# Optimization experiments

Measured on AMD Instinct MI355X. Metric: run time of the kernel, lower is better.

## Reference

```python
import jax, jax.numpy as jnp
import numpy as np

H, W = 128, 192          # image size (height, width) after imsz swap
K = 31                   # weight_sl (local window size)
T = K // 2               # replicate padding
C_FEAT = 64              # feat_dim
FFT_ROWS, FFT_COLS = 32, 48  # rect fft mask (after '48,32' swap)


def fft_rect(x):
    # rfft2 low-pass rectangular mask, exactly as fft_ifft with 'rect'.
    f = jnp.fft.rfft2(x)
    rows = jnp.arange(f.shape[-2])[:, None] < FFT_ROWS
    cols = jnp.arange(f.shape[-1])[None, :] < FFT_COLS
    f = f * (rows & cols)
    return jnp.fft.irfft2(f, s=x.shape[-2:])


def make_grid():
    t = float(T)  # weight_sl//2 with downsample_factor=1
    xs = jnp.linspace(-t, t, K)
    gx, gy = jnp.meshgrid(xs, xs, indexing='ij')
    return jnp.stack((gx, gy), axis=-1)  # [K,K,2]


def local_corr(src, tgt):
    # src, tgt: [C,H,W] -> cost volume [H,W,K,K]
    sp = jnp.pad(src, ((0, 0), (T, T), (T, T)), mode='edge')  # replicate pad
    rows = []
    for k in range(K):  # fixed structural loop over window rows
        sl = sp[:, k:k + H, :]  # [C,H,W+2T]
        win = jax.lax.conv_general_dilated_patches(sl[None], (1, K), (1, 1), 'VALID')[0]
        win = win.reshape(C_FEAT, K, H, W)  # [C,l,H,W]
        rows.append(jnp.einsum('chw,clhw->hwl', tgt, win))
    return jnp.stack(rows, axis=-2)  # [H,W,k,l]


def setup_inputs() -> dict:
    key = jax.random.key(0)
    k1, k2, k3 = jax.random.split(key, 3)
    fill_val = (1.0 / C_FEAT) ** 0.5
    feats = fill_val + 0.02 * jax.random.normal(k1, (1, 2, C_FEAT, H, W), jnp.float32)
    in_frames = jax.random.normal(k2, (1, 1, 3, H, W), jnp.float32)
    tgt_frames = jax.random.normal(k3, (1, 1, 3, H, W), jnp.float32)
    return {"in_frames": in_frames, "tgt_frames": tgt_frames, "feats": feats, "temp": 10}


def reference(in_frames, tgt_frames, feats, temp):
    # src_idx=0, tgt_idx=1, single-frame 'feats' path
    src = fft_rect(feats[0, 0])  # [C,H,W]
    tgt = fft_rect(feats[0, 1])
    # bilinear interpolate(scale_factor=1) is identity
    src = src / jnp.linalg.norm(src, axis=0, keepdims=True)
    tgt = tgt / jnp.linalg.norm(tgt, axis=0, keepdims=True)
    w = local_corr(src, tgt) * temp                       # [H,W,K,K]
    w = jax.nn.softmax(w.reshape(H, W, K * K), axis=-1).reshape(H, W, K, K)

    # windowed average of in_frames with per-pixel softmax weights
    xp = jnp.pad(in_frames[0, 0], ((0, 0), (T, T), (T, T)), mode='edge')
    patches = jax.lax.conv_general_dilated_patches(xp[None], (K, K), (1, 1), 'VALID')[0]
    patches = patches.reshape(3, K, K, H, W)              # [C,k,l,H,W]
    out = jnp.einsum('cklhw,hwkl->chw', patches, w)[None, None]  # [1,1,3,H,W]

    grid = make_grid()                                    # [K,K,2]
    pos = jnp.einsum('hwkl,klm->hwm', w, grid)[None, None]
    pos = pos[..., ::-1]                                  # .flip(-1)
    enorm = jnp.einsum('hwkl,kl->hw', w, jnp.linalg.norm(grid, axis=-1))[None, None]
    weights = w[None, None]                               # [1,1,H,W,K,K]
    return out, pos, enorm, weights
```

## Files before the change

### kernel.cpp

```cpp
#include <hip/hip_runtime.h>
#include <cstddef>

#define H 128
#define W 192
#define KS 31
#define CF 64
#define NPIX (H*W)
#define NKL (KS*KS)

#define OFF_POS (3*NPIX)
#define OFF_EN  (OFF_POS + 2*NPIX)
#define OFF_WGT (OFF_EN + NPIX)

#define NIMG NPIX
#define WS_CWT 0
#define WS_SWT 512
#define WS_CHT 1024
#define WS_SHT 1536
#define WS_U   2048
#define WS_Y   (WS_U + 2*128*NIMG)
#define WS_SN  (WS_Y + 128*NIMG)
#define WS_TN  (WS_SN + 32*NIMG)

#define PI_F 3.14159265358979323846f
#define ELS 962

typedef __attribute__((ext_vector_type(8))) short short8v;
typedef __attribute__((ext_vector_type(4))) float f32x4;

__device__ inline ushort bf16rtn(float f){
  uint u = __float_as_uint(f);
  u += 0x7fffu + ((u >> 16) & 1u);
  return (ushort)(u >> 16);
}
__device__ inline float bf2f(ushort h){ return __uint_as_float((uint)h << 16); }

__global__ __launch_bounds__(256) void k_tables(float* ws){
  int t = blockIdx.x*256 + threadIdx.x;
  if (t < 383){
    int d = t - 191;
    float c = 1.0f, s = 0.0f;
    for (int v = 1; v < 48; ++v){
      int m = (v*d) % 192; if (m < 0) m += 192;
      float a = (2.0f*PI_F/192.0f)*(float)m;
      c += 2.0f*cosf(a);
      s += 2.0f*sinf(a);
    }
    ws[WS_CWT + t] = c * (1.0f/192.0f);
    ws[WS_SWT + t] = s * (1.0f/192.0f);
  } else if (t < 383 + 255){
    int i = t - 383;
    int d = i - 127;
    float c = 0.0f, s = 0.0f;
    for (int u = 0; u < 32; ++u){
      int m = (u*d) % 128; if (m < 0) m += 128;
      float a = (2.0f*PI_F/128.0f)*(float)m;
      c += cosf(a);
      s += sinf(a);
    }
    ws[WS_CHT + i] = c * (1.0f/128.0f);
    ws[WS_SHT + i] = s * (1.0f/128.0f);
  }
}

__global__ __launch_bounds__(192) void k_colpass(const float* __restrict__ feats,
                                                const float* __restrict__ ws,
                                                float2* __restrict__ UV2){
  __shared__ float xs[16][192];
  __shared__ float tc[4][392], tn[4][392];
  int w  = threadIdx.x;
  int R0 = blockIdx.x * 16;
  for (int i = w; i < 380; i += 192){
#pragma unroll
    for (int s = 0; s < 4; ++s){
      tc[s][i] = ws[WS_CWT + i + s];
      tn[s][i] = ws[WS_SWT + i + s];
    }
  }
#pragma unroll
  for (int r = 0; r < 16; ++r) xs[r][w] = feats[(size_t)(R0 + r)*192 + w];
  __syncthreads();

  const int s = w & 3;
  const int boff = (w & ~3) + 188;
  const float* tcs = tc[s];
  const float* tns = tn[s];

  float u[16], v[16];
#pragma unroll
  for (int r = 0; r < 16; ++r){ u[r] = 0.0f; v[r] = 0.0f; }

  for (int wp0 = 0; wp0 < 192; wp0 += 4){
    const float4 cw4 = *reinterpret_cast<const float4*>(tcs + (boff - wp0));
    const float4 sw4 = *reinterpret_cast<const float4*>(tns + (boff - wp0));
#pragma unroll
    for (int r = 0; r < 16; ++r){
      const float4 x4 = *reinterpret_cast<const float4*>(&xs[r][wp0]);
      u[r] = fmaf(x4.x, cw4.w, u[r]);
      u[r] = fmaf(x4.y, cw4.z, u[r]);
      u[r] = fmaf(x4.z, cw4.y, u[r]);
      u[r] = fmaf(x4.w, cw4.x, u[r]);
      v[r] = fmaf(x4.x, sw4.w, v[r]);
      v[r] = fmaf(x4.y, sw4.z, v[r]);
      v[r] = fmaf(x4.z, sw4.y, v[r]);
      v[r] = fmaf(x4.w, sw4.x, v[r]);
    }
  }
#pragma unroll
  for (int r = 0; r < 16; ++r)
    UV2[(size_t)(R0 + r)*192 + w] = make_float2(u[r], v[r]);
}

__global__ __launch_bounds__(192) void k_rowpass(const float2* __restrict__ UV2,
                                                const float* __restrict__ ws,
                                                float* __restrict__ Y){
  __shared__ float Lc[4][144], Ls[4][144];
  int w = threadIdx.x;
  int ch = blockIdx.x >> 3;
  int h0 = (blockIdx.x & 7) * 16;
  for (int i = w; i < 143; i += 192){
#pragma unroll
    for (int s = 0; s < 4; ++s){
      int gi = h0 + i + s;
      Lc[s][i] = (gi < 255) ?  ws[WS_CHT + gi] : 0.0f;
      Ls[s][i] = (gi < 255) ? -ws[WS_SHT + gi] : 0.0f;
    }
  }
  __syncthreads();
  const float2* Uc = UV2 + (size_t)ch*NIMG;

  float acc[16];
#pragma unroll
  for (int r = 0; r < 16; ++r) acc[r] = 0.0f;

  for (int hp0 = 0; hp0 < 128; hp0 += 4){
    float2 uv0 = Uc[(hp0+0)*192 + w];
    float2 uv1 = Uc[(hp0+1)*192 + w];
    float2 uv2 = Uc[(hp0+2)*192 + w];
    float2 uv3 = Uc[(hp0+3)*192 + w];
#pragma unroll
    for (int r = 0; r < 16; ++r){
      int lb = 124 + (r & ~3) - hp0;
      const float4 c4 = *reinterpret_cast<const float4*>(&Lc[r & 3][lb]);
      const float4 s4 = *reinterpret_cast<const float4*>(&Ls[r & 3][lb]);
      acc[r] = fmaf(uv0.x, c4.w, acc[r]);
      acc[r] = fmaf(uv0.y, s4.w, acc[r]);
      acc[r] = fmaf(uv1.x, c4.z, acc[r]);
      acc[r] = fmaf(uv1.y, s4.z, acc[r]);
      acc[r] = fmaf(uv2.x, c4.y, acc[r]);
      acc[r] = fmaf(uv2.y, s4.y, acc[r]);
      acc[r] = fmaf(uv3.x, c4.x, acc[r]);
      acc[r] = fmaf(uv3.y, s4.x, acc[r]);
    }
  }
#pragma unroll
  for (int r = 0; r < 16; ++r)
    Y[(size_t)ch*NIMG + (h0 + r)*192 + w] = acc[r];
}

__global__ __launch_bounds__(192) void k_norm(const float* __restrict__ Y,
                                              ushort* __restrict__ SNh,
                                              ushort* __restrict__ TNh){
  int h = blockIdx.x, w = threadIdx.x;
  int which = blockIdx.y;
  int pix = h*192 + w;
  const float* base = Y + (size_t)which*64*NIMG + pix;
  float x[64];
  float ss = 0.0f;
#pragma unroll
  for (int c = 0; c < 64; ++c){
    x[c] = base[(size_t)c*NIMG];
    ss = fmaf(x[c], x[c], ss);
  }
  float rn = 1.0f / sqrtf(ss);
  ushort* o = (which ? TNh : SNh) + (size_t)pix*64;
#pragma unroll
  for (int q = 0; q < 8; ++q){
    ushort tmp[8];
#pragma unroll
    for (int e = 0; e < 8; ++e) tmp[e] = bf16rtn(x[q*8 + e] * rn);
    *reinterpret_cast<uint4*>(o + q*8) = *reinterpret_cast<const uint4*>(tmp);
  }
}

__global__ __launch_bounds__(256, 4) void k_corrsm(const ushort* __restrict__ SNh,
                                                   const ushort* __restrict__ TNh,
                                                   const int* __restrict__ temp,
                                                   const float* __restrict__ frames,
                                                   float* __restrict__ dout){
  __shared__ ushort eLu[16*ELS];
  __shared__ float red7[7][16][16];
  __shared__ float rsw[16];
  int h  = blockIdx.x;
  int bx = blockIdx.y;
  int t  = threadIdx.x;
  int lane = t & 63, wv = t >> 6;
  int n = lane & 15, g = lane >> 4;
  int w0 = bx * 16;
  float tempf = (float)(*temp);

  const ushort* ap = TNh + ((size_t)(h*192 + w0 + n))*64 + g*8;
  short8v a0 = *reinterpret_cast<const short8v*>(ap);
  short8v a1 = *reinterpret_cast<const short8v*>(ap + 32);

  for (int k = wv; k < KS; k += 4){
    int sh = h + k - 15; sh = sh < 0 ? 0 : (sh > 127 ? 127 : sh);
    const ushort* srow = SNh + (size_t)sh*192*64;
#pragma unroll
    for (int dj = 0; dj < 3; ++dj){
      int j0 = bx - 1 + dj;
      if (j0 < 0 || j0 > 11) continue;
      const ushort* bp = srow + ((size_t)(j0*16 + n))*64 + g*8;
      short8v b0 = *reinterpret_cast<const short8v*>(bp);
      short8v b1 = *reinterpret_cast<const short8v*>(bp + 32);
      f32x4 acc = {0.0f, 0.0f, 0.0f, 0.0f};
      acc = __builtin_amdgcn_mfma_f32_16x16x32_bf16(a0, b0, acc, 0, 0, 0);
      acc = __builtin_amdgcn_mfma_f32_16x16x32_bf16(a1, b1, acc, 0, 0, 0);
      int sx = j0*16 + n;
#pragma unroll
      for (int r = 0; r < 4; ++r){
        int wl = g*4 + r;
        int wg = w0 + wl;
        int l = sx - wg + 15;
        float e = __expf(acc[r]*tempf - tempf);
        ushort eb = bf16rtn(e);
        if (l >= 0 && l <= 30) eLu[wl*ELS + k*31 + l] = eb;
        if (bx == 0 && j0 == 0 && n == 0){
          for (int l2 = 0; l2 < 15 - wg; ++l2) eLu[wl*ELS + k*31 + l2] = eb;
        }
        if (bx == 11 && j0 == 11 && n == 15){
          for (int l2 = 207 - wg; l2 <= 30; ++l2) eLu[wl*ELS + k*31 + l2] = eb;
        }
      }
    }
  }
  __syncthreads();

  {
    float s=0, o0=0, o1=0, o2=0, p0=0, p1=0, en=0;
    int wl = t & 15;
    int wg = w0 + wl;
    for (int kk = t >> 4; kk < KS; kk += 16){
      int sh = h + kk - 15; sh = sh < 0 ? 0 : (sh > 127 ? 127 : sh);
      float dy = (float)(kk - 15);
      float dy2 = dy*dy;
      const float* f0p = frames + sh*192;
      const float* f1p = f0p + NPIX;
      const float* f2p = f0p + 2*NPIX;
      const ushort* src = eLu + wl*ELS + kk*31;
#pragma unroll
      for (int l = 0; l < KS; ++l){
        float e = bf2f(src[l]);
        float dx = (float)(l - 15);
        int ww = wg + l - 15; ww = ww < 0 ? 0 : (ww > 191 ? 191 : ww);
        s  += e;
        p0 = fmaf(e, dx, p0);
        p1 = fmaf(e, dy, p1);
        en = fmaf(e, sqrtf(dx*dx + dy2), en);
        o0 = fmaf(e, f0p[ww], o0);
        o1 = fmaf(e, f1p[ww], o1);
        o2 = fmaf(e, f2p[ww], o2);
      }
    }
    int q = t >> 4;
    red7[0][q][wl]=s;  red7[1][q][wl]=o0; red7[2][q][wl]=o1; red7[3][q][wl]=o2;
    red7[4][q][wl]=p0; red7[5][q][wl]=p1; red7[6][q][wl]=en;
  }
  __syncthreads();

  if (t < 16){
    float a[7];
#pragma unroll
    for (int j = 0; j < 7; ++j){
      float acc = 0.0f;
#pragma unroll
      for (int qq = 0; qq < 16; ++qq) acc += red7[j][qq][t];
      a[j] = acc;
    }
    float rs = 1.0f / a[0];
    int pix = h*192 + w0 + t;
    dout[0*NPIX + pix] = a[1]*rs;
    dout[1*NPIX + pix] = a[2]*rs;
    dout[2*NPIX + pix] = a[3]*rs;
    dout[OFF_POS + pix*2 + 0] = a[4]*rs;
    dout[OFF_POS + pix*2 + 1] = a[5]*rs;
    dout[OFF_EN + pix] = a[6]*rs;
    rsw[t] = rs;
  }
  __syncthreads();

#pragma unroll
  for (int rr = 0; rr < 4; ++rr){
    int row = wv*4 + rr;
    float rsv = rsw[row];
    float* dst = dout + OFF_WGT + ((size_t)(h*192 + w0 + row))*NKL;
    const ushort* src = eLu + row*ELS;
#pragma unroll
    for (int i = 0; i < 15; ++i){
      int j = i*64 + lane;
      __builtin_nontemporal_store(bf2f(src[j]) * rsv, dst + j);
    }
    if (lane == 0) __builtin_nontemporal_store(bf2f(src[960]) * rsv, dst + 960);
  }
}

extern "C" void kernel_launch(void* const* d_in, const int* in_sizes, int n_in,
                              void* d_out, int out_size, void* d_ws, size_t ws_size,
                              hipStream_t stream) {
  const float* frames = (const float*)d_in[0];
  const float* feats  = (const float*)d_in[2];
  const int*   temp   = (const int*)d_in[3];
  float* ws   = (float*)d_ws;
  float* dout = (float*)d_out;
  (void)in_sizes; (void)n_in; (void)out_size; (void)ws_size;

  float2* UV2 = (float2*)(ws + WS_U);
  float*  Y   = ws + WS_Y;
  ushort* SNh = (ushort*)(ws + WS_SN);
  ushort* TNh = (ushort*)(ws + WS_TN);

  hipLaunchKernelGGL(k_tables,  dim3(3),        dim3(256), 0, stream, ws);
  hipLaunchKernelGGL(k_colpass, dim3(1024),     dim3(192), 0, stream, feats, ws, UV2);
  hipLaunchKernelGGL(k_rowpass, dim3(1024),     dim3(192), 0, stream, UV2, ws, Y);
  hipLaunchKernelGGL(k_norm,    dim3(128, 2),   dim3(192), 0, stream, Y, SNh, TNh);
  hipLaunchKernelGGL(k_corrsm,  dim3(128, 12),  dim3(256), 0, stream, SNh, TNh, temp, frames, dout);
}
```

Before: 310.1 us.

## Swizzle softmax LDS layout, vectorize reads, shuffle-reduce, enlarge rowpass tiles

The exp buffer in LDS moves from a 31-element stride to 32-element segments with an XOR swizzle. The reduction phase can then read each 31-tap row as four 16-byte vector loads, and thread mapping changes so the 16 k-slots of one pixel sit in adjacent lanes. Those partials are combined with xor shuffles, which removes the shared-memory reduction array and one barrier. The rowpass kernel now computes 32 rows per block instead of 16, halving the grid and doubling register accumulators. The k_corrsm occupancy hint rises to 5 blocks per SM, which risks register spills.

New measurement: 446.8 us. +44.1%, slower.

```diff
diff --git a/kernel.cpp b/kernel.cpp
--- a/kernel.cpp
+++ b/kernel.cpp
@@ -23,7 +23,7 @@
 #define WS_TN  (WS_SN + 32*NIMG)
 
 #define PI_F 3.14159265358979323846f
-#define ELS 962
+#define SEG 32
 
 typedef __attribute__((ext_vector_type(8))) short short8v;
 typedef __attribute__((ext_vector_type(4))) float f32x4;
@@ -34,6 +34,7 @@
   return (ushort)(u >> 16);
 }
 __device__ inline float bf2f(ushort h){ return __uint_as_float((uint)h << 16); }
+__device__ inline int eidx(int X, int l){ return X*SEG + (l ^ (((X>>1)&3)<<3)); }
 
 __global__ __launch_bounds__(256) void k_tables(float* ws){
   int t = blockIdx.x*256 + threadIdx.x;
@@ -114,11 +115,11 @@
 __global__ __launch_bounds__(192) void k_rowpass(const float2* __restrict__ UV2,
                                                 const float* __restrict__ ws,
                                                 float* __restrict__ Y){
-  __shared__ float Lc[4][144], Ls[4][144];
+  __shared__ float Lc[4][160], Ls[4][160];
   int w = threadIdx.x;
-  int ch = blockIdx.x >> 3;
-  int h0 = (blockIdx.x & 7) * 16;
-  for (int i = w; i < 143; i += 192){
+  int ch = blockIdx.x >> 2;
+  int h0 = (blockIdx.x & 3) * 32;
+  for (int i = w; i < 156; i += 192){
 #pragma unroll
     for (int s = 0; s < 4; ++s){
       int gi = h0 + i + s;
@@ -129,9 +130,9 @@
   __syncthreads();
   const float2* Uc = UV2 + (size_t)ch*NIMG;
 
-  float acc[16];
-#pragma unroll
-  for (int r = 0; r < 16; ++r) acc[r] = 0.0f;
+  float acc[32];
+#pragma unroll
+  for (int r = 0; r < 32; ++r) acc[r] = 0.0f;
 
   for (int hp0 = 0; hp0 < 128; hp0 += 4){
     float2 uv0 = Uc[(hp0+0)*192 + w];
@@ -139,7 +140,7 @@
     float2 uv2 = Uc[(hp0+2)*192 + w];
     float2 uv3 = Uc[(hp0+3)*192 + w];
 #pragma unroll
-    for (int r = 0; r < 16; ++r){
+    for (int r = 0; r < 32; ++r){
       int lb = 124 + (r & ~3) - hp0;
       const float4 c4 = *reinterpret_cast<const float4*>(&Lc[r & 3][lb]);
       const float4 s4 = *reinterpret_cast<const float4*>(&Ls[r & 3][lb]);
@@ -154,7 +155,7 @@
     }
   }
 #pragma unroll
-  for (int r = 0; r < 16; ++r)
+  for (int r = 0; r < 32; ++r)
     Y[(size_t)ch*NIMG + (h0 + r)*192 + w] = acc[r];
 }
 
@@ -183,13 +184,12 @@
   }
 }
 
-__global__ __launch_bounds__(256, 4) void k_corrsm(const ushort* __restrict__ SNh,
+__global__ __launch_bounds__(256, 5) void k_corrsm(const ushort* __restrict__ SNh,
                                                    const ushort* __restrict__ TNh,
                                                    const int* __restrict__ temp,
                                                    const float* __restrict__ frames,
                                                    float* __restrict__ dout){
-  __shared__ ushort eLu[16*ELS];
-  __shared__ float red7[7][16][16];
+  __shared__ ushort eLu[16*KS*SEG];
   __shared__ float rsw[16];
   int h  = blockIdx.x;
   int bx = blockIdx.y;
@@ -224,12 +224,13 @@
         int l = sx - wg + 15;
         float e = __expf(acc[r]*tempf - tempf);
         ushort eb = bf16rtn(e);
-        if (l >= 0 && l <= 30) eLu[wl*ELS + k*31 + l] = eb;
+        int X = wl*KS + k;
+        if (l >= 0 && l <= 30) eLu[eidx(X, l)] = eb;
         if (bx == 0 && j0 == 0 && n == 0){
-          for (int l2 = 0; l2 < 15 - wg; ++l2) eLu[wl*ELS + k*31 + l2] = eb;
+          for (int l2 = 0; l2 < 15 - wg; ++l2) eLu[eidx(X, l2)] = eb;
         }
         if (bx == 11 && j0 == 11 && n == 15){
-          for (int l2 = 207 - wg; l2 <= 30; ++l2) eLu[wl*ELS + k*31 + l2] = eb;
+          for (int l2 = 207 - wg; l2 <= 30; ++l2) eLu[eidx(X, l2)] = eb;
         }
       }
     }
@@ -237,55 +238,65 @@
   __syncthreads();
 
   {
+    int wl = t >> 4, kslot = t & 15;
+    int wg = w0 + wl;
     float s=0, o0=0, o1=0, o2=0, p0=0, p1=0, en=0;
-    int wl = t & 15;
-    int wg = w0 + wl;
-    for (int kk = t >> 4; kk < KS; kk += 16){
+    for (int kk = kslot; kk < KS; kk += 16){
       int sh = h + kk - 15; sh = sh < 0 ? 0 : (sh > 127 ? 127 : sh);
       float dy = (float)(kk - 15);
       float dy2 = dy*dy;
       const float* f0p = frames + sh*192;
       const float* f1p = f0p + NPIX;
       const float* f2p = f0p + 2*NPIX;
-      const ushort* src = eLu + wl*ELS + kk*31;
-#pragma unroll
-      for (int l = 0; l < KS; ++l){
-        float e = bf2f(src[l]);
-        float dx = (float)(l - 15);
-        int ww = wg + l - 15; ww = ww < 0 ? 0 : (ww > 191 ? 191 : ww);
-        s  += e;
-        p0 = fmaf(e, dx, p0);
-        p1 = fmaf(e, dy, p1);
-        en = fmaf(e, sqrtf(dx*dx + dy2), en);
-        o0 = fmaf(e, f0p[ww], o0);
-        o1 = fmaf(e, f1p[ww], o1);
-        o2 = fmaf(e, f2p[ww], o2);
-      }
-    }
-    int q = t >> 4;
-    red7[0][q][wl]=s;  red7[1][q][wl]=o0; red7[2][q][wl]=o1; red7[3][q][wl]=o2;
-    red7[4][q][wl]=p0; red7[5][q][wl]=p1; red7[6][q][wl]=en;
-  }
-  __syncthreads();
-
-  if (t < 16){
-    float a[7];
-#pragma unroll
-    for (int j = 0; j < 7; ++j){
-      float acc = 0.0f;
-#pragma unroll
-      for (int qq = 0; qq < 16; ++qq) acc += red7[j][qq][t];
-      a[j] = acc;
-    }
-    float rs = 1.0f / a[0];
-    int pix = h*192 + w0 + t;
-    dout[0*NPIX + pix] = a[1]*rs;
-    dout[1*NPIX + pix] = a[2]*rs;
-    dout[2*NPIX + pix] = a[3]*rs;
-    dout[OFF_POS + pix*2 + 0] = a[4]*rs;
-    dout[OFF_POS + pix*2 + 1] = a[5]*rs;
-    dout[OFF_EN + pix] = a[6]*rs;
-    rsw[t] = rs;
+      int X = wl*KS + kk;
+      int sw8 = ((X>>1)&3) << 3;
+      const ushort* segp = eLu + X*SEG;
+      short8v e0 = *reinterpret_cast<const short8v*>(segp + (0  ^ sw8));
+      short8v e1 = *reinterpret_cast<const short8v*>(segp + (8  ^ sw8));
+      short8v e2 = *reinterpret_cast<const short8v*>(segp + (16 ^ sw8));
+      short8v e3 = *reinterpret_cast<const short8v*>(segp + (24 ^ sw8));
+#define TAP(l, vec, idx) { \
+      float e = bf2f((ushort)vec[idx]); \
+      float dx = (float)((l) - 15); \
+      int ww = wg + (l) - 15; ww = ww < 0 ? 0 : (ww > 191 ? 191 : ww); \
+      s += e; \
+      p0 = fmaf(e, dx, p0); \
+      p1 = fmaf(e, dy, p1); \
+      en = fmaf(e, sqrtf(dx*dx + dy2), en); \
+      o0 = fmaf(e, f0p[ww], o0); \
+      o1 = fmaf(e, f1p[ww], o1); \
+      o2 = fmaf(e, f2p[ww], o2); }
+      TAP(0,e0,0) TAP(1,e0,1) TAP(2,e0,2) TAP(3,e0,3)
+      TAP(4,e0,4) TAP(5,e0,5) TAP(6,e0,6) TAP(7,e0,7)
+      TAP(8,e1,0) TAP(9,e1,1) TAP(10,e1,2) TAP(11,e1,3)
+      TAP(12,e1,4) TAP(13,e1,5) TAP(14,e1,6) TAP(15,e1,7)
+      TAP(16,e2,0) TAP(17,e2,1) TAP(18,e2,2) TAP(19,e2,3)
+      TAP(20,e2,4) TAP(21,e2,5) TAP(22,e2,6) TAP(23,e2,7)
+      TAP(24,e3,0) TAP(25,e3,1) TAP(26,e3,2) TAP(27,e3,3)
+      TAP(28,e3,4) TAP(29,e3,5) TAP(30,e3,6)
+#undef TAP
+    }
+#pragma unroll
+    for (int mask = 1; mask <= 8; mask <<= 1){
+      s  += __shfl_xor(s,  mask);
+      o0 += __shfl_xor(o0, mask);
+      o1 += __shfl_xor(o1, mask);
+      o2 += __shfl_xor(o2, mask);
+      p0 += __shfl_xor(p0, mask);
+      p1 += __shfl_xor(p1, mask);
+      en += __shfl_xor(en, mask);
+    }
+    float rs = 1.0f / s;
+    if (kslot == 0){
+      int pix = h*192 + wg;
+      dout[0*NPIX + pix] = o0*rs;
+      dout[1*NPIX + pix] = o1*rs;
+      dout[2*NPIX + pix] = o2*rs;
+      dout[OFF_POS + pix*2 + 0] = p0*rs;
+      dout[OFF_POS + pix*2 + 1] = p1*rs;
+      dout[OFF_EN + pix] = en*rs;
+      rsw[wl] = rs;
+    }
   }
   __syncthreads();
 
@@ -294,13 +305,15 @@
     int row = wv*4 + rr;
     float rsv = rsw[row];
     float* dst = dout + OFF_WGT + ((size_t)(h*192 + w0 + row))*NKL;
-    const ushort* src = eLu + row*ELS;
 #pragma unroll
     for (int i = 0; i < 15; ++i){
       int j = i*64 + lane;
-      __builtin_nontemporal_store(bf2f(src[j]) * rsv, dst + j);
-    }
-    if (lane == 0) __builtin_nontemporal_store(bf2f(src[960]) * rsv, dst + 960);
+      int sg = j / 31;
+      int rem = j - sg*31;
+      __builtin_nontemporal_store(bf2f(eLu[eidx(row*KS + sg, rem)]) * rsv, dst + j);
+    }
+    if (lane == 0)
+      __builtin_nontemporal_store(bf2f(eLu[eidx(row*KS + 30, 30)]) * rsv, dst + 960);
   }
 }
 
@@ -321,7 +334,7 @@
 
   hipLaunchKernelGGL(k_tables,  dim3(3),        dim3(256), 0, stream, ws);
   hipLaunchKernelGGL(k_colpass, dim3(1024),     dim3(192), 0, stream, feats, ws, UV2);
-  hipLaunchKernelGGL(k_rowpass, dim3(1024),     dim3(192), 0, stream, UV2, ws, Y);
+  hipLaunchKernelGGL(k_rowpass, dim3(512),      dim3(192), 0, stream, UV2, ws, Y);
   hipLaunchKernelGGL(k_norm,    dim3(128, 2),   dim3(192), 0, stream, Y, SNh, TNh);
   hipLaunchKernelGGL(k_corrsm,  dim3(128, 12),  dim3(256), 0, stream, SNh, TNh, temp, frames, dout);
 }
```
